# Performance work log

Measured on AMD Instinct MI355X. Metric: run time of the kernel, lower is better.

## Reference

```python
import jax, jax.numpy as jnp
import numpy as np

HIDDEN = 2048
N_HEADS = 32
N_KV_HEADS = 8
HEAD_DIM = HIDDEN // N_HEADS  # 64
N_REP = N_HEADS // N_KV_HEADS  # 4
ROPE_THETA = 10000.0


def setup_inputs() -> dict:
    key = jax.random.key(0)
    ks = jax.random.split(key, 5)
    b, s = 2, 2048
    x = jax.random.normal(ks[0], (b, s, HIDDEN), dtype=jnp.float32)
    position_ids = jnp.arange(b * s, dtype=jnp.int32).reshape(b, s)
    sc = 1.0 / np.sqrt(HIDDEN)
    Wq = jax.random.normal(ks[1], (HIDDEN, HIDDEN), dtype=jnp.float32) * sc
    Wk = jax.random.normal(ks[2], (HIDDEN, N_KV_HEADS * HEAD_DIM), dtype=jnp.float32) * sc
    Wv = jax.random.normal(ks[3], (HIDDEN, N_KV_HEADS * HEAD_DIM), dtype=jnp.float32) * sc
    Wo = jax.random.normal(ks[4], (HIDDEN, HIDDEN), dtype=jnp.float32) * sc
    return {"input_ids": x, "Wq": Wq, "Wk": Wk, "Wv": Wv, "Wo": Wo,
            "position_ids": position_ids}


def _rope_cos_sin(position_ids, dtype):
    # inv_freq: [head_dim/2]
    inv_freq = 1.0 / (ROPE_THETA ** (jnp.arange(0, HEAD_DIM, 2, dtype=jnp.float32) / HEAD_DIM))
    freqs = position_ids.astype(jnp.float32)[..., None] * inv_freq  # [b, s, d/2]
    emb = jnp.concatenate([freqs, freqs], axis=-1)  # [b, s, d]
    return emb.astype(dtype), None  # placeholder, replaced below


def _rotate_half(x):
    x1, x2 = jnp.split(x, 2, axis=-1)
    return jnp.concatenate([-x2, x1], axis=-1)


def reference(input_ids, Wq, Wk, Wv, Wo, position_ids):
    b, s, _ = input_ids.shape
    q = (input_ids @ Wq).reshape(b, s, N_HEADS, HEAD_DIM).transpose(0, 2, 1, 3)      # [b,H,s,d]
    k = (input_ids @ Wk).reshape(b, s, N_KV_HEADS, HEAD_DIM).transpose(0, 2, 1, 3)   # [b,Hkv,s,d]
    v = (input_ids @ Wv).reshape(b, s, N_KV_HEADS, HEAD_DIM).transpose(0, 2, 1, 3)

    # RoPE
    inv_freq = 1.0 / (ROPE_THETA ** (jnp.arange(0, HEAD_DIM, 2, dtype=jnp.float32) / HEAD_DIM))
    freqs = position_ids.astype(jnp.float32)[..., None] * inv_freq  # [b,s,d/2]
    emb = jnp.concatenate([freqs, freqs], axis=-1)                   # [b,s,d]
    cos = jnp.cos(emb).astype(input_ids.dtype)[:, None, :, :]        # [b,1,s,d]
    sin = jnp.sin(emb).astype(input_ids.dtype)[:, None, :, :]
    q = q * cos + _rotate_half(q) * sin
    k = k * cos + _rotate_half(k) * sin

    # repeat_kv: [b,Hkv,s,d] -> [b,H,s,d]
    k = jnp.repeat(k, N_REP, axis=1)
    v = jnp.repeat(v, N_REP, axis=1)

    # causal SDPA
    scale = 1.0 / np.sqrt(HEAD_DIM)
    scores = jnp.einsum('bhqd,bhkd->bhqk', q, k) * scale
    causal = jnp.tril(jnp.ones((s, s), dtype=bool))
    scores = jnp.where(causal, scores, jnp.finfo(scores.dtype).min)
    attn = jax.nn.softmax(scores, axis=-1)
    out = jnp.einsum('bhqk,bhkd->bhqd', attn, v)                     # [b,H,s,d]
    out = out.transpose(0, 2, 1, 3).reshape(b, s, HIDDEN)
    return out @ Wo
```

## Files before the change

kernel.cpp:

```cpp
#include <hip/hip_runtime.h>
#include <hip/hip_bf16.h>

#define HIDDEN 2048
#define NHEADS 32
#define NKVH   8
#define HD     64
#define BATCH  2
#define SEQ    2048
#define ROWS   (BATCH * SEQ)
#define NQKV   3072
#define KCOL   2048
#define VCOL   2560

typedef __bf16 bf16x8 __attribute__((ext_vector_type(8)));
typedef __bf16 bf16x4 __attribute__((ext_vector_type(4)));
typedef float  f32x4  __attribute__((ext_vector_type(4)));
typedef short  s16x4  __attribute__((ext_vector_type(4)));
typedef short  s16x8  __attribute__((ext_vector_type(8)));

__device__ __forceinline__ void gl2lds16(const void* g, void* l) {
  __builtin_amdgcn_global_load_lds(
      (const __attribute__((address_space(1))) void*)g,
      (__attribute__((address_space(3))) void*)l, 16, 0, 0);
}

__device__ __forceinline__ short f2bs(float f) {
  __bf16 h = (__bf16)f;
  return __builtin_bit_cast(short, h);
}

__device__ __forceinline__ f32x4 mfma16(s16x4 a, s16x4 b, f32x4 c) {
#if __has_builtin(__builtin_amdgcn_mfma_f32_16x16x16bf16_1k)
  return __builtin_amdgcn_mfma_f32_16x16x16bf16_1k(a, b, c, 0, 0, 0);
#else
  s16x8 a8 = __builtin_shufflevector(a, (s16x4){0,0,0,0}, 0,1,2,3,4,5,6,7);
  s16x8 b8 = __builtin_shufflevector(b, (s16x4){0,0,0,0}, 0,1,2,3,4,5,6,7);
  a8[4]=0;a8[5]=0;a8[6]=0;a8[7]=0; b8[4]=0;b8[5]=0;b8[6]=0;b8[7]=0;
  return __builtin_amdgcn_mfma_f32_16x16x32_bf16(
      __builtin_bit_cast(bf16x8, a8), __builtin_bit_cast(bf16x8, b8), c, 0, 0, 0);
#endif
}

__global__ void prep(const float* __restrict__ Wq, const float* __restrict__ Wk,
                     const float* __restrict__ Wv, const float* __restrict__ Wo,
                     const float* __restrict__ x,
                     __bf16* __restrict__ dstW, __bf16* __restrict__ Xb) {
  __shared__ __bf16 tile[32][33];
  int bid = blockIdx.x, tid = threadIdx.x;
  if (bid < 10240) {
    int n0 = (bid % 160) * 32, k0 = (bid / 160) * 32;
    int tx = tid & 31, ty = tid >> 5;
    const float* src;
    int N, c0;
    if (n0 < 2048)      { src = Wq; N = 2048; c0 = n0; }
    else if (n0 < 2560) { src = Wk; N = 512;  c0 = n0 - 2048; }
    else if (n0 < 3072) { src = Wv; N = 512;  c0 = n0 - 2560; }
    else                { src = Wo; N = 2048; c0 = n0 - 3072; }
#pragma unroll
    for (int i = 0; i < 32; i += 8)
      tile[ty + i][tx] = (__bf16)src[(size_t)(k0 + ty + i) * N + (c0 + tx)];
    __syncthreads();
#pragma unroll
    for (int i = 0; i < 32; i += 8)
      dstW[(size_t)(n0 + ty + i) * HIDDEN + (k0 + tx)] = tile[tx][ty + i];
  } else {
    size_t i = (size_t)(bid - 10240) * 256 + tid;
    const float4* s = (const float4*)(x + i * 16);
    float4 a = s[0], b = s[1], c = s[2], d = s[3];
    bf16x8 o0, o1;
    o0[0] = (__bf16)a.x; o0[1] = (__bf16)a.y; o0[2] = (__bf16)a.z; o0[3] = (__bf16)a.w;
    o0[4] = (__bf16)b.x; o0[5] = (__bf16)b.y; o0[6] = (__bf16)b.z; o0[7] = (__bf16)b.w;
    o1[0] = (__bf16)c.x; o1[1] = (__bf16)c.y; o1[2] = (__bf16)c.z; o1[3] = (__bf16)c.w;
    o1[4] = (__bf16)d.x; o1[5] = (__bf16)d.y; o1[6] = (__bf16)d.z; o1[7] = (__bf16)d.w;
    *(bf16x8*)(Xb + i * 16)     = o0;
    *(bf16x8*)(Xb + i * 16 + 8) = o1;
  }
}

template <typename OutT, bool ROPE>
__launch_bounds__(256, 2)
__global__ void gemm_bt(const __bf16* __restrict__ A, const __bf16* __restrict__ Bt,
                        OutT* __restrict__ C, int M, int N, int K,
                        const int* __restrict__ pos_ids, __bf16* __restrict__ Vt) {
  __shared__ __bf16 As[2][128 * 32];
  __shared__ __bf16 Bs[2][128 * 32];
  int id = blockIdx.x;
  int bm = (id & 7) * 4 + ((id >> 3) & 3);
  int bn = id >> 5;
  int t = threadIdx.x;
  int wave = t >> 6, lane = t & 63, l16 = lane & 15, quad = lane >> 4;
  int wm = (wave >> 1) * 64, wn = (wave & 1) * 64;

  f32x4 acc[4][4] = {};

  int arow = t >> 2;
  int ac   = (t & 3) * 8;
  const __bf16* Ag = A  + (size_t)(bm * 128 + arow) * K + ac;
  const __bf16* Bg = Bt + (size_t)(bn * 128 + arow) * K + ac;
  int woff = wave * 512;

  for (int k0 = 0; k0 < K; k0 += 64) {
    __syncthreads();
    gl2lds16(Ag + k0,                      &As[0][woff]);
    gl2lds16(Ag + (size_t)64 * K + k0,      &As[0][2048 + woff]);
    gl2lds16(Ag + k0 + 32,                 &As[1][woff]);
    gl2lds16(Ag + (size_t)64 * K + k0 + 32, &As[1][2048 + woff]);
    gl2lds16(Bg + k0,                      &Bs[0][woff]);
    gl2lds16(Bg + (size_t)64 * K + k0,      &Bs[0][2048 + woff]);
    gl2lds16(Bg + k0 + 32,                 &Bs[1][woff]);
    gl2lds16(Bg + (size_t)64 * K + k0 + 32, &Bs[1][2048 + woff]);
    __syncthreads();

#pragma unroll
    for (int ks = 0; ks < 2; ++ks) {
      bf16x8 af[4], bfr[4];
#pragma unroll
      for (int i = 0; i < 4; ++i) {
        af[i]  = *(const bf16x8*)(&As[ks][(wm + i * 16 + l16) * 32 + quad * 8]);
        bfr[i] = *(const bf16x8*)(&Bs[ks][(wn + i * 16 + l16) * 32 + quad * 8]);
      }
#pragma unroll
      for (int i = 0; i < 4; ++i)
#pragma unroll
        for (int j = 0; j < 4; ++j)
          acc[i][j] = __builtin_amdgcn_mfma_f32_16x16x32_bf16(af[i], bfr[j], acc[i][j], 0, 0, 0);
    }
  }

  if (ROPE) {
    int headidx = bn * 2 + (wn >> 6);
    if (headidx >= 40) {
#pragma unroll
      for (int i = 0; i < 4; ++i) {
        int srow = bm * 128 + wm + i * 16 + quad * 4;
        int b = srow >> 11, s = srow & 2047;
#pragma unroll
        for (int j = 0; j < 4; ++j) {
          int vcol = bn * 128 + wn + j * 16 + l16 - VCOL;
          int hk = vcol >> 6, d = vcol & 63;
          bf16x4 w;
#pragma unroll
          for (int r = 0; r < 4; ++r) w[r] = (__bf16)acc[i][j][r];
          *(bf16x4*)(Vt + ((size_t)(b * NKVH + hk) * HD + d) * SEQ + s) = w;
        }
      }
      return;
    }
    float invrev0 = __expf(-(float)l16 * 0.28782313662425574f) * 0.15915494309189535f;
    float invrev1 = __expf(-(float)(l16 + 16) * 0.28782313662425574f) * 0.15915494309189535f;
#pragma unroll
    for (int i = 0; i < 4; ++i)
#pragma unroll
      for (int r = 0; r < 4; ++r) {
        int gr = bm * 128 + wm + i * 16 + quad * 4 + r;
        float pos = (float)pos_ids[gr];
        float rv0 = pos * invrev0; rv0 -= floorf(rv0);
        float rv1 = pos * invrev1; rv1 -= floorf(rv1);
        float a0 = rv0 * 6.283185307179586f, a1 = rv1 * 6.283185307179586f;
        float s0 = __sinf(a0), c0 = __cosf(a0);
        float s1 = __sinf(a1), c1 = __cosf(a1);
        float x0 = acc[i][0][r], x2 = acc[i][2][r];
        acc[i][0][r] = x0 * c0 - x2 * s0;
        acc[i][2][r] = x2 * c0 + x0 * s0;
        float x1 = acc[i][1][r], x3 = acc[i][3][r];
        acc[i][1][r] = x1 * c1 - x3 * s1;
        acc[i][3][r] = x3 * c1 + x1 * s1;
      }
  }

#pragma unroll
  for (int i = 0; i < 4; ++i)
#pragma unroll
    for (int j = 0; j < 4; ++j)
#pragma unroll
      for (int r = 0; r < 4; ++r)
        C[(size_t)(bm * 128 + wm + i * 16 + quad * 4 + r) * N +
          (bn * 128 + wn + j * 16 + l16)] = (OutT)acc[i][j][r];
}

__launch_bounds__(256, 3)
__global__ void flash_attn(const __bf16* __restrict__ QKV, const __bf16* __restrict__ Vt,
                           __bf16* __restrict__ O) {
  int p = blockIdx.x >> 1, h2 = blockIdx.x & 1;
  int hk = blockIdx.y, b = blockIdx.z;
  int t = threadIdx.x;
  int wave = t >> 6, lane = t & 63, l16 = lane & 15, quad = lane >> 4;
  int hh = h2 * 2 + (wave >> 1);
  int h  = hk * 4 + hh;
  int qs = wave & 1;

  __shared__ __bf16 Ks[2][2][64 * 32];
  __shared__ __bf16 Vs[2][4096];

  const __bf16* Kbase = QKV + (size_t)(b * SEQ) * NQKV + KCOL + hk * HD;
  const __bf16* VtB   = Vt + (size_t)(b * NKVH + hk) * HD * SEQ;

  int kr = wave * 16 + (lane >> 2);
  int kc = (lane & 3) * 8;
  int vd = wave * 16 + (lane >> 2);
  int vsc = (lane & 3) * 16;
  int vs4w = (lane & 3) * 4;

  for (int seg = 0; seg < 2; ++seg) {
    int qt = seg ? (31 - p) : p;

    __syncthreads();

    bf16x8 qfrag[2][2];
#pragma unroll
    for (int qi = 0; qi < 2; ++qi) {
      const __bf16* qp = QKV + (size_t)(b * SEQ + qt * 64 + qs * 32 + qi * 16 + l16) * NQKV
                       + h * HD + quad * 8;
      bf16x8 q0 = *(const bf16x8*)qp;
      bf16x8 q1 = *(const bf16x8*)(qp + 32);
#pragma unroll
      for (int e = 0; e < 8; ++e) {
        qfrag[qi][0][e] = (__bf16)((float)q0[e] * 0.125f);
        qfrag[qi][1][e] = (__bf16)((float)q1[e] * 0.125f);
      }
    }

    float lsum[2] = {0.f, 0.f};
    f32x4 oacc[2][4];
#pragma unroll
    for (int qi = 0; qi < 2; ++qi)
#pragma unroll
      for (int dt = 0; dt < 4; ++dt) oacc[qi][dt] = (f32x4){0.f, 0.f, 0.f, 0.f};

    {
      const __bf16* kp = Kbase + (size_t)kr * NQKV + kc;
      gl2lds16(kp,      &Ks[0][0][wave * 512]);
      gl2lds16(kp + 32, &Ks[0][1][wave * 512]);
      const __bf16* vp = VtB + (size_t)vd * SEQ + vsc;
      s16x8 v0 = __builtin_bit_cast(s16x8, *(const bf16x8*)vp);
      s16x8 v1 = __builtin_bit_cast(s16x8, *(const bf16x8*)(vp + 8));
      *(s16x4*)(&Vs[0][(vs4w + 0) * 256 + vd * 4]) = __builtin_shufflevector(v0, v0, 0, 1, 2, 3);
      *(s16x4*)(&Vs[0][(vs4w + 1) * 256 + vd * 4]) = __builtin_shufflevector(v0, v0, 4, 5, 6, 7);
      *(s16x4*)(&Vs[0][(vs4w + 2) * 256 + vd * 4]) = __builtin_shufflevector(v1, v1, 0, 1, 2, 3);
      *(s16x4*)(&Vs[0][(vs4w + 3) * 256 + vd * 4]) = __builtin_shufflevector(v1, v1, 4, 5, 6, 7);
    }

    for (int kt = 0; kt <= qt; ++kt) {
      int buf = kt & 1;
      __syncthreads();

      bool pre = (kt < qt);
      s16x8 pv0, pv1;
      if (pre) {
        const __bf16* kp = Kbase + (size_t)((kt + 1) * 64 + kr) * NQKV + kc;
        gl2lds16(kp,      &Ks[buf ^ 1][0][wave * 512]);
        gl2lds16(kp + 32, &Ks[buf ^ 1][1][wave * 512]);
        const __bf16* vp = VtB + (size_t)vd * SEQ + (kt + 1) * 64 + vsc;
        pv0 = __builtin_bit_cast(s16x8, *(const bf16x8*)vp);
        pv1 = __builtin_bit_cast(s16x8, *(const bf16x8*)(vp + 8));
      }

      f32x4 sacc[2][4];
#pragma unroll
      for (int qi = 0; qi < 2; ++qi)
#pragma unroll
        for (int nt = 0; nt < 4; ++nt) sacc[qi][nt] = (f32x4){0.f, 0.f, 0.f, 0.f};
#pragma unroll
      for (int ks = 0; ks < 2; ++ks) {
        bf16x8 kf[4];
#pragma unroll
        for (int nt = 0; nt < 4; ++nt)
          kf[nt] = *(const bf16x8*)(&Ks[buf][ks][(nt * 16 + l16) * 32 + quad * 8]);
#pragma unroll
        for (int nt = 0; nt < 4; ++nt)
#pragma unroll
          for (int qi = 0; qi < 2; ++qi)
            sacc[qi][nt] = __builtin_amdgcn_mfma_f32_16x16x32_bf16(kf[nt], qfrag[qi][ks], sacc[qi][nt], 0, 0, 0);
      }

      s16x4 af[2][4];
      if (kt == qt) {
#pragma unroll
        for (int qi = 0; qi < 2; ++qi)
#pragma unroll
          for (int nt = 0; nt < 4; ++nt)
#pragma unroll
            for (int r = 0; r < 4; ++r) {
              int kg = nt * 16 + quad * 4 + r;
              int qg = qs * 32 + qi * 16 + l16;
              float e = __expf((kg > qg) ? -1e30f : sacc[qi][nt][r]);
              lsum[qi] += e;
              af[qi][nt][r] = f2bs(e);
            }
      } else {
#pragma unroll
        for (int qi = 0; qi < 2; ++qi)
#pragma unroll
          for (int nt = 0; nt < 4; ++nt)
#pragma unroll
            for (int r = 0; r < 4; ++r) {
              float e = __expf(sacc[qi][nt][r]);
              lsum[qi] += e;
              af[qi][nt][r] = f2bs(e);
            }
      }

#pragma unroll
      for (int nt = 0; nt < 4; ++nt) {
        s16x4 vf[4];
#pragma unroll
        for (int dt = 0; dt < 4; ++dt)
          vf[dt] = *(const s16x4*)(&Vs[buf][(nt * 4 + quad) * 256 + (dt * 16 + l16) * 4]);
#pragma unroll
        for (int qi = 0; qi < 2; ++qi)
#pragma unroll
          for (int dt = 0; dt < 4; ++dt)
            oacc[qi][dt] = mfma16(af[qi][nt], vf[dt], oacc[qi][dt]);
      }

      if (pre) {
        *(s16x4*)(&Vs[buf ^ 1][(vs4w + 0) * 256 + vd * 4]) = __builtin_shufflevector(pv0, pv0, 0, 1, 2, 3);
        *(s16x4*)(&Vs[buf ^ 1][(vs4w + 1) * 256 + vd * 4]) = __builtin_shufflevector(pv0, pv0, 4, 5, 6, 7);
        *(s16x4*)(&Vs[buf ^ 1][(vs4w + 2) * 256 + vd * 4]) = __builtin_shufflevector(pv1, pv1, 0, 1, 2, 3);
        *(s16x4*)(&Vs[buf ^ 1][(vs4w + 3) * 256 + vd * 4]) = __builtin_shufflevector(pv1, pv1, 4, 5, 6, 7);
      }
    }

#pragma unroll
    for (int qi = 0; qi < 2; ++qi) {
      float l = lsum[qi];
      l += __shfl_xor(l, 16);
      l += __shfl_xor(l, 32);
#pragma unroll
      for (int r = 0; r < 4; ++r) {
        float lr = __shfl(l, quad * 4 + r);
        float inv = 1.0f / lr;
#pragma unroll
        for (int dt = 0; dt < 4; ++dt) {
          float o = oacc[qi][dt][r] * inv;
          O[(size_t)(b * SEQ + qt * 64 + qs * 32 + qi * 16 + quad * 4 + r) * HIDDEN +
            h * HD + dt * 16 + l16] = (__bf16)o;
        }
      }
    }
  }
}

extern "C" void kernel_launch(void* const* d_in, const int* in_sizes, int n_in,
                              void* d_out, int out_size, void* d_ws, size_t ws_size,
                              hipStream_t stream) {
  const float* x  = (const float*)d_in[0];
  const float* Wq = (const float*)d_in[1];
  const float* Wk = (const float*)d_in[2];
  const float* Wv = (const float*)d_in[3];
  const float* Wo = (const float*)d_in[4];
  const int* pos  = (const int*)d_in[5];

  __bf16* Wqkvt = (__bf16*)d_ws;
  __bf16* Wot   = Wqkvt + (size_t)NQKV * HIDDEN;
  __bf16* Xb    = Wot + (size_t)HIDDEN * HIDDEN;
  __bf16* QKV   = Xb + (size_t)ROWS * HIDDEN;
  __bf16* Oat   = QKV + (size_t)ROWS * NQKV;
  __bf16* Vt    = Xb;

  prep<<<dim3(12288), 256, 0, stream>>>(Wq, Wk, Wv, Wo, x, Wqkvt, Xb);

  gemm_bt<__bf16, true><<<dim3(768), 256, 0, stream>>>(
      Xb, Wqkvt, QKV, ROWS, NQKV, HIDDEN, pos, Vt);

  flash_attn<<<dim3(32, NKVH, BATCH), 256, 0, stream>>>(QKV, Vt, Oat);

  gemm_bt<float, false><<<dim3(512), 256, 0, stream>>>(
      Oat, Wot, (float*)d_out, ROWS, HIDDEN, HIDDEN, nullptr, nullptr);
}
```

Before: 268.8 us.

## Split attention into one block per q-tile, read V from global, sum via MFMA

Replaces the paired causal q-tile scheme (each block handling tiles p and 31-p) with one block per q-tile, launched longest-first over a 1024-block 1D grid for dynamic load balance. The V LDS staging buffer is removed: V fragments are loaded directly from global memory each iteration. The row sum is computed with an extra MFMA against a ones vector instead of scalar adds and cross-lane shuffles. This removes LDS traffic and reduction shuffles and improves scheduling, but risks uncoalesced global V loads and extra MFMA work.

```diff
diff --git a/kernel.cpp b/kernel.cpp
--- a/kernel.cpp
+++ b/kernel.cpp
@@ -181,8 +181,10 @@
 __launch_bounds__(256, 3)
 __global__ void flash_attn(const __bf16* __restrict__ QKV, const __bf16* __restrict__ Vt,
                            __bf16* __restrict__ O) {
-  int p = blockIdx.x >> 1, h2 = blockIdx.x & 1;
-  int hk = blockIdx.y, b = blockIdx.z;
+  int x = blockIdx.x;
+  int qt = 31 - (x >> 5);
+  int c = x & 31;
+  int h2 = c & 1, hk = (c >> 1) & 7, b = c >> 4;
   int t = threadIdx.x;
   int wave = t >> 6, lane = t & 63, l16 = lane & 15, quad = lane >> 4;
   int hh = h2 * 2 + (wave >> 1);
@@ -190,155 +192,124 @@
   int qs = wave & 1;
 
   __shared__ __bf16 Ks[2][2][64 * 32];
-  __shared__ __bf16 Vs[2][4096];
 
   const __bf16* Kbase = QKV + (size_t)(b * SEQ) * NQKV + KCOL + hk * HD;
   const __bf16* VtB   = Vt + (size_t)(b * NKVH + hk) * HD * SEQ;
 
   int kr = wave * 16 + (lane >> 2);
   int kc = (lane & 3) * 8;
-  int vd = wave * 16 + (lane >> 2);
-  int vsc = (lane & 3) * 16;
-  int vs4w = (lane & 3) * 4;
-
-  for (int seg = 0; seg < 2; ++seg) {
-    int qt = seg ? (31 - p) : p;
-
+
+  bf16x8 qfrag[2][2];
+#pragma unroll
+  for (int qi = 0; qi < 2; ++qi) {
+    const __bf16* qp = QKV + (size_t)(b * SEQ + qt * 64 + qs * 32 + qi * 16 + l16) * NQKV
+                     + h * HD + quad * 8;
+    bf16x8 q0 = *(const bf16x8*)qp;
+    bf16x8 q1 = *(const bf16x8*)(qp + 32);
+#pragma unroll
+    for (int e = 0; e < 8; ++e) {
+      qfrag[qi][0][e] = (__bf16)((float)q0[e] * 0.125f);
+      qfrag[qi][1][e] = (__bf16)((float)q1[e] * 0.125f);
+    }
+  }
+
+  f32x4 oacc[2][4], oaccl[2];
+#pragma unroll
+  for (int qi = 0; qi < 2; ++qi) {
+    oaccl[qi] = (f32x4){0.f, 0.f, 0.f, 0.f};
+#pragma unroll
+    for (int dt = 0; dt < 4; ++dt) oacc[qi][dt] = (f32x4){0.f, 0.f, 0.f, 0.f};
+  }
+
+  const s16x4 vones = {(short)0x3F80, (short)0x3F80, (short)0x3F80, (short)0x3F80};
+
+  {
+    const __bf16* kp = Kbase + (size_t)kr * NQKV + kc;
+    gl2lds16(kp,      &Ks[0][0][wave * 512]);
+    gl2lds16(kp + 32, &Ks[0][1][wave * 512]);
+  }
+
+  for (int kt = 0; kt <= qt; ++kt) {
+    int buf = kt & 1;
     __syncthreads();
 
-    bf16x8 qfrag[2][2];
-#pragma unroll
-    for (int qi = 0; qi < 2; ++qi) {
-      const __bf16* qp = QKV + (size_t)(b * SEQ + qt * 64 + qs * 32 + qi * 16 + l16) * NQKV
-                       + h * HD + quad * 8;
-      bf16x8 q0 = *(const bf16x8*)qp;
-      bf16x8 q1 = *(const bf16x8*)(qp + 32);
-#pragma unroll
-      for (int e = 0; e < 8; ++e) {
-        qfrag[qi][0][e] = (__bf16)((float)q0[e] * 0.125f);
-        qfrag[qi][1][e] = (__bf16)((float)q1[e] * 0.125f);
-      }
-    }
-
-    float lsum[2] = {0.f, 0.f};
-    f32x4 oacc[2][4];
+    if (kt < qt) {
+      const __bf16* kp = Kbase + (size_t)((kt + 1) * 64 + kr) * NQKV + kc;
+      gl2lds16(kp,      &Ks[buf ^ 1][0][wave * 512]);
+      gl2lds16(kp + 32, &Ks[buf ^ 1][1][wave * 512]);
+    }
+
+    s16x4 vf[4][4];
+#pragma unroll
+    for (int nt = 0; nt < 4; ++nt)
+#pragma unroll
+      for (int dt = 0; dt < 4; ++dt)
+        vf[nt][dt] = *(const s16x4*)(VtB + (size_t)(dt * 16 + l16) * SEQ
+                                     + kt * 64 + nt * 16 + quad * 4);
+
+    f32x4 sacc[2][4];
 #pragma unroll
     for (int qi = 0; qi < 2; ++qi)
 #pragma unroll
-      for (int dt = 0; dt < 4; ++dt) oacc[qi][dt] = (f32x4){0.f, 0.f, 0.f, 0.f};
-
-    {
-      const __bf16* kp = Kbase + (size_t)kr * NQKV + kc;
-      gl2lds16(kp,      &Ks[0][0][wave * 512]);
-      gl2lds16(kp + 32, &Ks[0][1][wave * 512]);
-      const __bf16* vp = VtB + (size_t)vd * SEQ + vsc;
-      s16x8 v0 = __builtin_bit_cast(s16x8, *(const bf16x8*)vp);
-      s16x8 v1 = __builtin_bit_cast(s16x8, *(const bf16x8*)(vp + 8));
-      *(s16x4*)(&Vs[0][(vs4w + 0) * 256 + vd * 4]) = __builtin_shufflevector(v0, v0, 0, 1, 2, 3);
-      *(s16x4*)(&Vs[0][(vs4w + 1) * 256 + vd * 4]) = __builtin_shufflevector(v0, v0, 4, 5, 6, 7);
-      *(s16x4*)(&Vs[0][(vs4w + 2) * 256 + vd * 4]) = __builtin_shufflevector(v1, v1, 0, 1, 2, 3);
-      *(s16x4*)(&Vs[0][(vs4w + 3) * 256 + vd * 4]) = __builtin_shufflevector(v1, v1, 4, 5, 6, 7);
-    }
-
-    for (int kt = 0; kt <= qt; ++kt) {
-      int buf = kt & 1;
-      __syncthreads();
-
-      bool pre = (kt < qt);
-      s16x8 pv0, pv1;
-      if (pre) {
-        const __bf16* kp = Kbase + (size_t)((kt + 1) * 64 + kr) * NQKV + kc;
-        gl2lds16(kp,      &Ks[buf ^ 1][0][wave * 512]);
-        gl2lds16(kp + 32, &Ks[buf ^ 1][1][wave * 512]);
-        const __bf16* vp = VtB + (size_t)vd * SEQ + (kt + 1) * 64 + vsc;
-        pv0 = __builtin_bit_cast(s16x8, *(const bf16x8*)vp);
-        pv1 = __builtin_bit_cast(s16x8, *(const bf16x8*)(vp + 8));
-      }
-
-      f32x4 sacc[2][4];
+      for (int nt = 0; nt < 4; ++nt) sacc[qi][nt] = (f32x4){0.f, 0.f, 0.f, 0.f};
+#pragma unroll
+    for (int ks = 0; ks < 2; ++ks) {
+      bf16x8 kf[4];
+#pragma unroll
+      for (int nt = 0; nt < 4; ++nt)
+        kf[nt] = *(const bf16x8*)(&Ks[buf][ks][(nt * 16 + l16) * 32 + quad * 8]);
+#pragma unroll
+      for (int nt = 0; nt < 4; ++nt)
+#pragma unroll
+        for (int qi = 0; qi < 2; ++qi)
+          sacc[qi][nt] = __builtin_amdgcn_mfma_f32_16x16x32_bf16(kf[nt], qfrag[qi][ks], sacc[qi][nt], 0, 0, 0);
+    }
+
+    s16x4 af[2][4];
+    if (kt == qt) {
 #pragma unroll
       for (int qi = 0; qi < 2; ++qi)
 #pragma unroll
-        for (int nt = 0; nt < 4; ++nt) sacc[qi][nt] = (f32x4){0.f, 0.f, 0.f, 0.f};
-#pragma unroll
-      for (int ks = 0; ks < 2; ++ks) {
-        bf16x8 kf[4];
-#pragma unroll
         for (int nt = 0; nt < 4; ++nt)
-          kf[nt] = *(const bf16x8*)(&Ks[buf][ks][(nt * 16 + l16) * 32 + quad * 8]);
+#pragma unroll
+          for (int r = 0; r < 4; ++r) {
+            int kg = nt * 16 + quad * 4 + r;
+            int qg = qs * 32 + qi * 16 + l16;
+            af[qi][nt][r] = f2bs(__expf((kg > qg) ? -1e30f : sacc[qi][nt][r]));
+          }
+    } else {
+#pragma unroll
+      for (int qi = 0; qi < 2; ++qi)
 #pragma unroll
         for (int nt = 0; nt < 4; ++nt)
 #pragma unroll
-          for (int qi = 0; qi < 2; ++qi)
-            sacc[qi][nt] = __builtin_amdgcn_mfma_f32_16x16x32_bf16(kf[nt], qfrag[qi][ks], sacc[qi][nt], 0, 0, 0);
-      }
-
-      s16x4 af[2][4];
-      if (kt == qt) {
-#pragma unroll
-        for (int qi = 0; qi < 2; ++qi)
-#pragma unroll
-          for (int nt = 0; nt < 4; ++nt)
-#pragma unroll
-            for (int r = 0; r < 4; ++r) {
-              int kg = nt * 16 + quad * 4 + r;
-              int qg = qs * 32 + qi * 16 + l16;
-              float e = __expf((kg > qg) ? -1e30f : sacc[qi][nt][r]);
-              lsum[qi] += e;
-              af[qi][nt][r] = f2bs(e);
-            }
-      } else {
-#pragma unroll
-        for (int qi = 0; qi < 2; ++qi)
-#pragma unroll
-          for (int nt = 0; nt < 4; ++nt)
-#pragma unroll
-            for (int r = 0; r < 4; ++r) {
-              float e = __expf(sacc[qi][nt][r]);
-              lsum[qi] += e;
-              af[qi][nt][r] = f2bs(e);
-            }
-      }
-
-#pragma unroll
-      for (int nt = 0; nt < 4; ++nt) {
-        s16x4 vf[4];
+          for (int r = 0; r < 4; ++r)
+            af[qi][nt][r] = f2bs(__expf(sacc[qi][nt][r]));
+    }
+
+#pragma unroll
+    for (int nt = 0; nt < 4; ++nt)
+#pragma unroll
+      for (int qi = 0; qi < 2; ++qi) {
+        oaccl[qi] = mfma16(af[qi][nt], vones, oaccl[qi]);
 #pragma unroll
         for (int dt = 0; dt < 4; ++dt)
-          vf[dt] = *(const s16x4*)(&Vs[buf][(nt * 4 + quad) * 256 + (dt * 16 + l16) * 4]);
-#pragma unroll
-        for (int qi = 0; qi < 2; ++qi)
-#pragma unroll
-          for (int dt = 0; dt < 4; ++dt)
-            oacc[qi][dt] = mfma16(af[qi][nt], vf[dt], oacc[qi][dt]);
-      }
-
-      if (pre) {
-        *(s16x4*)(&Vs[buf ^ 1][(vs4w + 0) * 256 + vd * 4]) = __builtin_shufflevector(pv0, pv0, 0, 1, 2, 3);
-        *(s16x4*)(&Vs[buf ^ 1][(vs4w + 1) * 256 + vd * 4]) = __builtin_shufflevector(pv0, pv0, 4, 5, 6, 7);
-        *(s16x4*)(&Vs[buf ^ 1][(vs4w + 2) * 256 + vd * 4]) = __builtin_shufflevector(pv1, pv1, 0, 1, 2, 3);
-        *(s16x4*)(&Vs[buf ^ 1][(vs4w + 3) * 256 + vd * 4]) = __builtin_shufflevector(pv1, pv1, 4, 5, 6, 7);
-      }
-    }
-
-#pragma unroll
-    for (int qi = 0; qi < 2; ++qi) {
-      float l = lsum[qi];
-      l += __shfl_xor(l, 16);
-      l += __shfl_xor(l, 32);
-#pragma unroll
-      for (int r = 0; r < 4; ++r) {
-        float lr = __shfl(l, quad * 4 + r);
-        float inv = 1.0f / lr;
-#pragma unroll
-        for (int dt = 0; dt < 4; ++dt) {
-          float o = oacc[qi][dt][r] * inv;
-          O[(size_t)(b * SEQ + qt * 64 + qs * 32 + qi * 16 + quad * 4 + r) * HIDDEN +
-            h * HD + dt * 16 + l16] = (__bf16)o;
-        }
-      }
-    }
-  }
+          oacc[qi][dt] = mfma16(af[qi][nt], vf[nt][dt], oacc[qi][dt]);
+      }
+  }
+
+#pragma unroll
+  for (int qi = 0; qi < 2; ++qi)
+#pragma unroll
+    for (int r = 0; r < 4; ++r) {
+      float inv = 1.0f / oaccl[qi][r];
+#pragma unroll
+      for (int dt = 0; dt < 4; ++dt) {
+        float o = oacc[qi][dt][r] * inv;
+        O[(size_t)(b * SEQ + qt * 64 + qs * 32 + qi * 16 + quad * 4 + r) * HIDDEN +
+          h * HD + dt * 16 + l16] = (__bf16)o;
+      }
+    }
 }
 
 extern "C" void kernel_launch(void* const* d_in, const int* in_sizes, int n_in,
@@ -363,7 +334,7 @@
   gemm_bt<__bf16, true><<<dim3(768), 256, 0, stream>>>(
       Xb, Wqkvt, QKV, ROWS, NQKV, HIDDEN, pos, Vt);
 
-  flash_attn<<<dim3(32, NKVH, BATCH), 256, 0, stream>>>(QKV, Vt, Oat);
+  flash_attn<<<dim3(1024), 256, 0, stream>>>(QKV, Vt, Oat);
 
   gemm_bt<float, false><<<dim3(512), 256, 0, stream>>>(
       Oat, Wot, (float*)d_out, ROWS, HIDDEN, HIDDEN, nullptr, nullptr);
```

Result: slower. 350.4 us (+30.4%).
